# Kernel optimization log

Hardware: AMD Instinct MI355X
Metric: run time of the kernel (lower is better)

Reference implementation:

```python
import jax, jax.numpy as jnp
import numpy as np
import math

D_K = 64
ROUNDS = 4
BUCKET_LEN = 64


def _l2norm(x, axis):
    n = jnp.sqrt(jnp.sum(x * x, axis=axis, keepdims=True))
    return x / jnp.maximum(n, 1e-12)


def _look_back(x):
    # x: (B, n_buckets, bucket_len, ...) -> (B, n_buckets, 2*bucket_len, ...)
    # each bucket is concatenated with the previous bucket (wrapping at 0)
    shift = jnp.concatenate([x[:, -1:], x[:, :-1]], axis=1)
    return jnp.concatenate([shift, x], axis=2)


def _lsh_hash(query, rand_matrix):
    # returns position-tagged hashes: bucket_id * L + position, shape (B, L, R)
    B, L, D = query.shape
    qn = _l2norm(query, -1)
    rm = _l2norm(rand_matrix, 1)  # normalize over d_k dim, as in torch code
    xR = jnp.einsum('bld,bdrn->blrn', qn, rm)
    h = jnp.argmax(jnp.concatenate([xR, -xR], axis=-1), axis=-1).astype(jnp.int32)
    return h * L + jnp.arange(L, dtype=jnp.int32)[None, :, None]


def _attend(query, value, hash_indice, original_indice, sorted_hashes):
    B, L, D = query.shape
    nb = L // BUCKET_LEN
    R = ROUNDS
    # gather queries into hash-sorted order, per round: (B, L, D, R)
    rq = jnp.take_along_axis(query[:, :, :, None], hash_indice[:, :, None, :], axis=1)
    rq = rq.reshape(B, nb, BUCKET_LEN, D, R)
    lk = _l2norm(_look_back(rq), -2)  # keys = normalized lookback queries (shared QK)
    qk = jnp.einsum('bnijk,bnljk->bnilk', rq, lk) / math.sqrt(D_K)  # (B,nb,bl,2bl,R)
    # mask cross-bucket pairs
    sh = (sorted_hashes // L).reshape(B, nb, BUCKET_LEN, R)
    qk = jnp.where(sh[..., None, :] != _look_back(sh)[..., None, :, :], -1e9, qk)
    # mask self-attention (causal=False so no causal mask)
    qi = hash_indice.reshape(B, nb, BUCKET_LEN, R).astype(jnp.int32)
    ki = _look_back(qi)
    qk = jnp.where(qi[..., None, :] == ki[..., None, :, :], -1e5, qk)
    qk = qk.reshape(B, L, 2 * BUCKET_LEN, R)
    lse = jax.scipy.special.logsumexp(qk, axis=2)  # (B, L, R)
    p = jnp.exp(qk - lse[:, :, None, :]).reshape(B, nb, BUCKET_LEN, 2 * BUCKET_LEN, R)
    # gather values into sorted order and apply lookback attention
    rv = jnp.take_along_axis(value[:, :, :, None], hash_indice[:, :, None, :], axis=1)
    rv = rv.reshape(B, nb, BUCKET_LEN, D, R)
    att = jnp.einsum('bnijl,bnjkl->bnikl', p, _look_back(rv)).reshape(B, L, D, R)
    # scatter back to original order
    att = jnp.take_along_axis(att, original_indice[:, :, None, :], axis=1)
    lse = jnp.take_along_axis(lse, original_indice, axis=1)
    # NOTE: faithful to source, softmax over dim=1 (sequence dim)
    w = jax.nn.softmax(lse, axis=1)  # (B, L, R)
    return jnp.einsum('blir,blr->bli', att, w)  # (B, L, D)


def setup_inputs() -> dict:
    key = jax.random.key(0)
    k1, k2, k3 = jax.random.split(key, 3)
    B, L, D = 16, 8192, D_K
    n_buckets = L // BUCKET_LEN
    return {
        'query': jax.random.normal(k1, (B, L, D), jnp.float32),
        'value': jax.random.normal(k2, (B, L, D), jnp.float32),
        'rand_matrix': jax.random.normal(k3, (B, D, ROUNDS, n_buckets // 2), jnp.float32),
    }


def reference(query, value, rand_matrix):
    hashes = _lsh_hash(query, rand_matrix)          # (B, L, R) int32
    hash_indice = jnp.argsort(hashes, axis=1)       # sort positions by hash
    sorted_hashes = jnp.take_along_axis(hashes, hash_indice, axis=1)
    original_indice = jnp.argsort(hash_indice, axis=1)  # inverse permutation
    return _attend(query, value, hash_indice.astype(jnp.int32),
                   original_indice.astype(jnp.int32), sorted_hashes)
```

## Files before the change

### kernel.cpp

```cpp
#include <hip/hip_runtime.h>
#include <math.h>

#define B_   16
#define L_   8192
#define D_   64
#define R_   4
#define NB_  128
#define NH_  64

typedef float v2f __attribute__((ext_vector_type(2)));

__device__ __forceinline__ float dpp_xor1(float x) {
    return __int_as_float(__builtin_amdgcn_mov_dpp(__float_as_int(x), 0xB1, 0xf, 0xf, true));
}
__device__ __forceinline__ float dpp_xor2(float x) {
    return __int_as_float(__builtin_amdgcn_mov_dpp(__float_as_int(x), 0x4E, 0xf, 0xf, true));
}
__device__ __forceinline__ float quad_bcast0(float x) {
    return __int_as_float(__builtin_amdgcn_mov_dpp(__float_as_int(x), 0x00, 0xf, 0xf, true));
}
__device__ __forceinline__ float quad_bcast1(float x) {
    return __int_as_float(__builtin_amdgcn_mov_dpp(__float_as_int(x), 0x55, 0xf, 0xf, true));
}
__device__ __forceinline__ float quad_bcast2(float x) {
    return __int_as_float(__builtin_amdgcn_mov_dpp(__float_as_int(x), 0xAA, 0xf, 0xf, true));
}
__device__ __forceinline__ float quad_bcast3(float x) {
    return __int_as_float(__builtin_amdgcn_mov_dpp(__float_as_int(x), 0xFF, 0xf, 0xf, true));
}

__global__ __launch_bounds__(64) void k_rmnorm(const float* __restrict__ rm, double* __restrict__ rmn) {
    int b = blockIdx.x >> 2, r = blockIdx.x & 3;
    int n = threadIdx.x;
    float v[D_];
    double ss = 0.0;
    #pragma unroll
    for (int d = 0; d < D_; ++d) {
        float f = rm[((size_t)(b * D_ + d) * R_ + r) * NH_ + n];
        v[d] = f;
        ss += (double)f * (double)f;
    }
    double nrm = sqrt(ss); if (nrm < 1e-12) nrm = 1e-12;
    double inv = 1.0 / nrm;
    double* o = rmn + ((size_t)(b * R_ + r) * NH_ + n) * D_;
    #pragma unroll
    for (int d = 0; d < D_; ++d) o[d] = (double)v[d] * inv;
}

__global__ __launch_bounds__(256) void k_hash(const float* __restrict__ q, const double* __restrict__ rmn,
                                              float* __restrict__ rn, int* __restrict__ h) {
    __shared__ double rmd[NH_ * D_];
    __shared__ float  rms[NH_ * D_];
    int b = blockIdx.z, r = blockIdx.y;
    int l = blockIdx.x * 256 + threadIdx.x;
    const double* src = rmn + (size_t)(b * R_ + r) * NH_ * D_;
    for (int i = threadIdx.x; i < NH_ * D_; i += 256) {
        double dv = src[i];
        rmd[i] = dv;
        rms[i] = (float)dv;
    }
    const float* qp = q + ((size_t)b * L_ + l) * D_;
    v2f qv2[D_ / 2];
    double ss = 0.0;
    #pragma unroll
    for (int d = 0; d < D_; d += 4) {
        float4 f = *(const float4*)(qp + d);
        qv2[d >> 1]       = (v2f){f.x, f.y};
        qv2[(d >> 1) + 1] = (v2f){f.z, f.w};
        ss += (double)f.x * f.x + (double)f.y * f.y + (double)f.z * f.z + (double)f.w * f.w;
    }
    __syncthreads();
    float best = -1.0e30f, second = -1.0e30f; int bi = 0;
    for (int n = 0; n < NH_; ++n) {
        const float* kp = &rms[n * D_];
        v2f a0 = (v2f){0.f, 0.f}, a1 = a0;
        #pragma unroll
        for (int d = 0; d < D_; d += 4) {
            float4 kk = *(const float4*)(kp + d);
            a0 = __builtin_elementwise_fma(qv2[d >> 1],       (v2f){kk.x, kk.y}, a0);
            a1 = __builtin_elementwise_fma(qv2[(d >> 1) + 1], (v2f){kk.z, kk.w}, a1);
        }
        float s = (a0.x + a0.y) + (a1.x + a1.y);
        if (s > best)       { second = best; best = s; bi = n; }
        else if (s > second)  second = s;
        float ns = -s;
        if (ns > best)      { second = best; best = ns; bi = n + NH_; }
        else if (ns > second) second = ns;
    }
    float qn = (float)sqrt(ss);
    if (best - second < 1.2e-5f * qn + 1.0e-7f) {
        double qd[D_];
        #pragma unroll
        for (int d = 0; d < D_; d += 2) {
            qd[d] = (double)qv2[d >> 1].x; qd[d + 1] = (double)qv2[d >> 1].y;
        }
        double bestd = -1.0e300; bi = 0;
        for (int n = 0; n < NH_; ++n) {
            const double* kp = &rmd[n * D_];
            double a0 = 0, a1 = 0, a2 = 0, a3 = 0;
            #pragma unroll
            for (int d = 0; d < D_; d += 4) {
                a0 = fma(qd[d],   kp[d],   a0);
                a1 = fma(qd[d+1], kp[d+1], a1);
                a2 = fma(qd[d+2], kp[d+2], a2);
                a3 = fma(qd[d+3], kp[d+3], a3);
            }
            double s = (a0 + a1) + (a2 + a3);
            if (s > bestd)  { bestd = s;  bi = n; }
            if (-s > bestd) { bestd = -s; bi = n + NH_; }
        }
    }
    h[(size_t)(b * R_ + r) * L_ + l] = bi;
    if (r == 0) {
        double nrm = sqrt(ss); if (nrm < 1e-12) nrm = 1e-12;
        rn[(size_t)b * L_ + l] = (float)(1.0 / nrm);
    }
}

__global__ __launch_bounds__(64) void k_sort(const int* __restrict__ h, int* __restrict__ idx,
                                             int* __restrict__ sb, int* __restrict__ iv) {
    __shared__ unsigned int cnt[NB_ * 64];
    int br = blockIdx.x;
    const int* hh = h + (size_t)br * L_;
    int t = threadIdx.x;
    for (int i = t; i < NB_ * 64; i += 64) cnt[i] = 0;
    __syncthreads();
    int base = t * 128;
    for (int i = 0; i < 128; ++i) { int bk = hh[base + i]; cnt[bk * 64 + t]++; }
    __syncthreads();
    int fb = t * 128;
    unsigned int local = 0;
    for (int i = 0; i < 128; ++i) local += cnt[fb + i];
    unsigned int v = local;
    #pragma unroll
    for (int off = 1; off < 64; off <<= 1) {
        unsigned int u = __shfl_up(v, off);
        if (t >= off) v += u;
    }
    unsigned int run = v - local;
    for (int i = 0; i < 128; ++i) { unsigned int c0 = cnt[fb + i]; cnt[fb + i] = run; run += c0; }
    __syncthreads();
    int* oi = idx + (size_t)br * L_;
    int* ob = sb  + (size_t)br * L_;
    int* ivp = iv + (size_t)br * L_;
    for (int i = 0; i < 128; ++i) {
        int l = base + i; int bk = hh[l];
        unsigned int pos = cnt[bk * 64 + t]++;
        oi[pos] = l; ob[pos] = bk; ivp[l] = (int)pos;
    }
}

__global__ __launch_bounds__(128) void k_flash(const float* __restrict__ q, const float* __restrict__ val,
                                               const int* __restrict__ idx, const int* __restrict__ sb,
                                               const float* __restrict__ rn, float* __restrict__ lse,
                                               const float* __restrict__ gm, const float* __restrict__ gs,
                                               float* __restrict__ out, float* __restrict__ contrib,
                                               int r_fixed, int omode) {
    __shared__ float kt[2][16 * 80];
    __shared__ float vt[2][16 * 80];
    __shared__ int   kqs[2][16];
    __shared__ int   kbs[2][16];
    __shared__ float krs[2][16];
    int w   = threadIdx.x >> 6;
    int tid = threadIdx.x & 63;
    int c = blockIdx.x * 2 + w, b = blockIdx.z;
    int r = (r_fixed < 0) ? (int)blockIdx.y : r_fixed;
    size_t sbase = (size_t)(b * R_ + r) * L_;
    int h = tid & 3;
    int posq = c * 64 + (tid >> 2) * 4;
    int mls[4];
    #pragma unroll
    for (int qq = 0; qq < 4; ++qq) mls[qq] = idx[sbase + posq + qq];
    int ownpos  = posq + h;
    int myl_own = idx[sbase + ownpos];
    int mybk_own = sb[sbase + ownpos];
    float m_own = 0.125f / rn[(size_t)b * L_ + myl_own];
    const float* qb = q   + (size_t)b * L_ * D_;
    const float* vb = val + (size_t)b * L_ * D_;
    v2f qv2[4][8];
    #pragma unroll
    for (int qq = 0; qq < 4; ++qq) {
        const float* qp = qb + (size_t)mls[qq] * D_ + h * 16;
        #pragma unroll
        for (int i = 0; i < 16; i += 4) {
            float4 f = *(const float4*)(qp + i);
            qv2[qq][i >> 1]       = (v2f){f.x, f.y};
            qv2[qq][(i >> 1) + 1] = (v2f){f.z, f.w};
        }
    }
    float ps[4] = {0.0f, 0.0f, 0.0f, 0.0f};
    v2f acc2[4][8];
    #pragma unroll
    for (int qq = 0; qq < 4; ++qq)
        #pragma unroll
        for (int i = 0; i < 8; ++i) acc2[qq][i] = (v2f){0.0f, 0.0f};

    #pragma unroll 1
    for (int s = 0; s < 8; ++s) {
        int ck = ((c + NB_ - 1 + (s >> 2)) & (NB_ - 1)) * 64 + (s & 3) * 16;
        {
            int rw = tid >> 2, cc = tid & 3;
            int kl = idx[sbase + ck + rw];
            const float* kp = qb + (size_t)kl * D_ + cc * 16;
            float* kd = &kt[w][rw * 80 + cc * 20];
            #pragma unroll
            for (int i = 0; i < 16; i += 4) *(float4*)(kd + i) = *(const float4*)(kp + i);
            if (omode != 2) {
                const float* vp = vb + (size_t)kl * D_ + cc * 16;
                float* vd = &vt[w][rw * 80 + cc * 20];
                #pragma unroll
                for (int i = 0; i < 16; i += 4) *(float4*)(vd + i) = *(const float4*)(vp + i);
            }
            if (tid < 16) {
                int kl2 = idx[sbase + ck + tid];
                kqs[w][tid] = kl2;
                kbs[w][tid] = sb[sbase + ck + tid];
                krs[w][tid] = rn[(size_t)b * L_ + kl2] * 0.125f;
            }
        }
        #pragma unroll
        for (int j = 0; j < 16; ++j) {
            const float* kpj = &kt[w][j * 80 + h * 20];
            v2f a0 = (v2f){0.f, 0.f}, a1 = a0, a2 = a0, a3 = a0;
            #pragma unroll
            for (int i = 0; i < 16; i += 4) {
                float4 kk = *(const float4*)(kpj + i);
                v2f kA = (v2f){kk.x, kk.y}, kB = (v2f){kk.z, kk.w};
                int i2 = i >> 1;
                a0 = __builtin_elementwise_fma(qv2[0][i2], kA, a0);
                a0 = __builtin_elementwise_fma(qv2[0][i2 + 1], kB, a0);
                a1 = __builtin_elementwise_fma(qv2[1][i2], kA, a1);
                a1 = __builtin_elementwise_fma(qv2[1][i2 + 1], kB, a1);
                a2 = __builtin_elementwise_fma(qv2[2][i2], kA, a2);
                a2 = __builtin_elementwise_fma(qv2[2][i2 + 1], kB, a2);
                a3 = __builtin_elementwise_fma(qv2[3][i2], kA, a3);
                a3 = __builtin_elementwise_fma(qv2[3][i2 + 1], kB, a3);
            }
            float p0 = a0.x + a0.y, p1 = a1.x + a1.y, p2 = a2.x + a2.y, p3 = a3.x + a3.y;
            bool b0 = (h & 1), b1 = (h & 2) != 0;
            float u0 = b0 ? p1 : p0;
            float t0 = b0 ? p0 : p1;
            u0 += dpp_xor1(t0);
            float u2 = b0 ? p3 : p2;
            float t2 = b0 ? p2 : p3;
            u2 += dpp_xor1(t2);
            float dot = b1 ? u2 : u0;
            float t3 = b1 ? u0 : u2;
            dot += dpp_xor2(t3);
            float sc = dot * krs[w][j];
            sc = (kbs[w][j] == mybk_own) ? sc : -1.0e9f;
            if (kqs[w][j] == myl_own) sc = -1.0e5f;
            float p = __expf(sc - m_own);
            ps[j & 3] += p;
            if (omode != 2) {
                v2f P0 = (v2f){quad_bcast0(p), quad_bcast0(p)};
                v2f P1 = (v2f){quad_bcast1(p), quad_bcast1(p)};
                v2f P2 = (v2f){quad_bcast2(p), quad_bcast2(p)};
                v2f P3 = (v2f){quad_bcast3(p), quad_bcast3(p)};
                const float* vpj = &vt[w][j * 80 + h * 20];
                #pragma unroll
                for (int i = 0; i < 16; i += 4) {
                    float4 vv = *(const float4*)(vpj + i);
                    v2f vA = (v2f){vv.x, vv.y}, vB = (v2f){vv.z, vv.w};
                    int i2 = i >> 1;
                    acc2[0][i2]     = __builtin_elementwise_fma(P0, vA, acc2[0][i2]);
                    acc2[0][i2 + 1] = __builtin_elementwise_fma(P0, vB, acc2[0][i2 + 1]);
                    acc2[1][i2]     = __builtin_elementwise_fma(P1, vA, acc2[1][i2]);
                    acc2[1][i2 + 1] = __builtin_elementwise_fma(P1, vB, acc2[1][i2 + 1]);
                    acc2[2][i2]     = __builtin_elementwise_fma(P2, vA, acc2[2][i2]);
                    acc2[2][i2 + 1] = __builtin_elementwise_fma(P2, vB, acc2[2][i2 + 1]);
                    acc2[3][i2]     = __builtin_elementwise_fma(P3, vA, acc2[3][i2]);
                    acc2[3][i2 + 1] = __builtin_elementwise_fma(P3, vB, acc2[3][i2 + 1]);
                }
            }
        }
    }
    float sum = (ps[0] + ps[1]) + (ps[2] + ps[3]);
    float lse_own, inv_own;
    if (sum > 0.0f) { lse_own = m_own + logf(sum); inv_own = 1.0f / sum; }
    else            { lse_own = -3.0e38f;          inv_own = 0.0f; }
    if (omode != 3) lse[sbase + ownpos] = lse_own;
    if (omode == 0 || omode == 1) {
        float ivs[4];
        ivs[0] = quad_bcast0(inv_own); ivs[1] = quad_bcast1(inv_own);
        ivs[2] = quad_bcast2(inv_own); ivs[3] = quad_bcast3(inv_own);
        float* cbase = contrib + ((omode == 0) ? (size_t)(b * R_ + r) * L_ : (size_t)b * L_) * D_;
        #pragma unroll
        for (int qq = 0; qq < 4; ++qq) {
            float* cp = cbase + (size_t)(posq + qq) * D_ + h * 16;
            #pragma unroll
            for (int i = 0; i < 16; i += 4) {
                int i2 = i >> 1;
                float4 o;
                o.x = acc2[qq][i2].x * ivs[qq];     o.y = acc2[qq][i2].y * ivs[qq];
                o.z = acc2[qq][i2 + 1].x * ivs[qq]; o.w = acc2[qq][i2 + 1].y * ivs[qq];
                *(float4*)(cp + i) = o;
            }
        }
    } else if (omode == 3) {
        int brr = b * R_ + r;
        float gmv = gm[brr], gsv = gs[brr];
        float ls4[4], iv4[4];
        ls4[0] = quad_bcast0(lse_own); ls4[1] = quad_bcast1(lse_own);
        ls4[2] = quad_bcast2(lse_own); ls4[3] = quad_bcast3(lse_own);
        iv4[0] = quad_bcast0(inv_own); iv4[1] = quad_bcast1(inv_own);
        iv4[2] = quad_bcast2(inv_own); iv4[3] = quad_bcast3(inv_own);
        #pragma unroll
        for (int qq = 0; qq < 4; ++qq) {
            float wq = __expf(ls4[qq] - gmv) * gsv * iv4[qq];
            float* op = out + ((size_t)b * L_ + mls[qq]) * D_ + h * 16;
            #pragma unroll
            for (int i = 0; i < 8; ++i) {
                unsafeAtomicAdd(op + 2 * i,     wq * acc2[qq][i].x);
                unsafeAtomicAdd(op + 2 * i + 1, wq * acc2[qq][i].y);
            }
        }
    }
}

__global__ __launch_bounds__(256) void k_wred(const float* __restrict__ lse, float* __restrict__ gm,
                                              float* __restrict__ gs, int r_w) {
    __shared__ float  sm[4];
    __shared__ double sd[4];
    int br = (r_w < 0) ? (int)blockIdx.x : ((int)blockIdx.x * R_ + r_w);
    const float* x = lse + (size_t)br * L_;
    int t = threadIdx.x;
    float mx = -3.0e38f;
    for (int i = t; i < L_; i += 256) mx = fmaxf(mx, x[i]);
    #pragma unroll
    for (int o = 32; o; o >>= 1) mx = fmaxf(mx, __shfl_down(mx, o));
    if ((t & 63) == 0) sm[t >> 6] = mx;
    __syncthreads();
    mx = fmaxf(fmaxf(sm[0], sm[1]), fmaxf(sm[2], sm[3]));
    double s = 0.0;
    for (int i = t; i < L_; i += 256) s += exp((double)x[i] - (double)mx);
    #pragma unroll
    for (int o = 32; o; o >>= 1) s += __shfl_down(s, o);
    if ((t & 63) == 0) sd[t >> 6] = s;
    __syncthreads();
    if (t == 0) { gm[br] = mx; gs[br] = (float)(1.0 / (sd[0] + sd[1] + sd[2] + sd[3])); }
}

__global__ __launch_bounds__(256) void k_comb_full(const float* __restrict__ contrib,
                                                   const int* __restrict__ iv,
                                                   const float* __restrict__ lse,
                                                   const float* __restrict__ gm,
                                                   const float* __restrict__ gs,
                                                   float* __restrict__ out) {
    int gid = blockIdx.x * 256 + threadIdx.x;
    int row = gid >> 2;
    int ch  = (gid & 3) * 16;
    int b = row >> 13, l = row & (L_ - 1);
    float s[16];
    #pragma unroll
    for (int i = 0; i < 16; ++i) s[i] = 0.0f;
    #pragma unroll
    for (int r = 0; r < R_; ++r) {
        int brr = b * R_ + r;
        int pos = iv[(size_t)brr * L_ + l];
        float w = expf(lse[(size_t)brr * L_ + pos] - gm[brr]) * gs[brr];
        const float* cp = contrib + ((size_t)brr * L_ + pos) * D_ + ch;
        #pragma unroll
        for (int i = 0; i < 16; i += 4) {
            float4 f = *(const float4*)(cp + i);
            s[i]   = fmaf(w, f.x, s[i]);   s[i+1] = fmaf(w, f.y, s[i+1]);
            s[i+2] = fmaf(w, f.z, s[i+2]); s[i+3] = fmaf(w, f.w, s[i+3]);
        }
    }
    float* op = out + (size_t)row * D_ + ch;
    #pragma unroll
    for (int i = 0; i < 16; i += 4) {
        float4 o; o.x = s[i]; o.y = s[i+1]; o.z = s[i+2]; o.w = s[i+3];
        *(float4*)(op + i) = o;
    }
}

__global__ __launch_bounds__(256) void k_comb_add(const float* __restrict__ contrib,
                                                  const int* __restrict__ iv,
                                                  const float* __restrict__ lse,
                                                  const float* __restrict__ gm,
                                                  const float* __restrict__ gs,
                                                  float* __restrict__ out, int r) {
    int gid = blockIdx.x * 256 + threadIdx.x;
    int row = gid >> 2;
    int ch  = (gid & 3) * 16;
    int b = row >> 13, l = row & (L_ - 1);
    int brr = b * R_ + r;
    int pos = iv[(size_t)brr * L_ + l];
    float w = expf(lse[(size_t)brr * L_ + pos] - gm[brr]) * gs[brr];
    const float* cp = contrib + ((size_t)b * L_ + pos) * D_ + ch;
    float* op = out + (size_t)row * D_ + ch;
    #pragma unroll
    for (int i = 0; i < 16; i += 4) {
        float4 f = *(const float4*)(cp + i);
        float4 o = *(const float4*)(op + i);
        o.x = fmaf(w, f.x, o.x); o.y = fmaf(w, f.y, o.y);
        o.z = fmaf(w, f.z, o.z); o.w = fmaf(w, f.w, o.w);
        *(float4*)(op + i) = o;
    }
}

#define OFF_RMN     0u
#define OFF_RN      2097152u
#define OFF_H       2621440u
#define OFF_IDX     4718592u
#define OFF_SB      6815744u
#define OFF_LSE     8912896u
#define OFF_GM      11010048u
#define OFF_GS      11010304u
#define OFF_INV     11010560u
#define OFF_CONTRIB 13107712u
#define CONTRIB_FULL_BYTES  134217728ull
#define CONTRIB_SLICE_BYTES 33554432ull

extern "C" void kernel_launch(void* const* d_in, const int* in_sizes, int n_in,
                              void* d_out, int out_size, void* d_ws, size_t ws_size,
                              hipStream_t stream) {
    const float* q  = (const float*)d_in[0];
    const float* v  = (const float*)d_in[1];
    const float* rm = (const float*)d_in[2];
    float* out = (float*)d_out;
    char* ws = (char*)d_ws;
    double* rmn = (double*)(ws + OFF_RMN);
    float*  rn  = (float*)(ws + OFF_RN);
    int*    h   = (int*)(ws + OFF_H);
    int*    idx = (int*)(ws + OFF_IDX);
    int*    sb  = (int*)(ws + OFF_SB);
    float*  lse = (float*)(ws + OFF_LSE);
    float*  gm  = (float*)(ws + OFF_GM);
    float*  gs  = (float*)(ws + OFF_GS);
    int*    iv  = (int*)(ws + OFF_INV);
    float*  contrib = (float*)(ws + OFF_CONTRIB);

    int tierA = (ws_size >= (size_t)OFF_CONTRIB + CONTRIB_FULL_BYTES) ? 1 : 0;
    int tierB = (!tierA && ws_size >= (size_t)OFF_CONTRIB + CONTRIB_SLICE_BYTES) ? 1 : 0;

    hipLaunchKernelGGL(k_rmnorm, dim3(B_ * R_), dim3(64), 0, stream, rm, rmn);
    hipLaunchKernelGGL(k_hash, dim3(L_ / 256, R_, B_), dim3(256), 0, stream, q, rmn, rn, h);
    hipLaunchKernelGGL(k_sort, dim3(B_ * R_), dim3(64), 0, stream, h, idx, sb, iv);

    if (tierA) {
        hipLaunchKernelGGL(k_flash, dim3(NB_ / 2, R_, B_), dim3(128), 0, stream, q, v, idx, sb, rn,
                           lse, gm, gs, out, contrib, -1, 0);
        hipLaunchKernelGGL(k_wred, dim3(B_ * R_), dim3(256), 0, stream, lse, gm, gs, -1);
        hipLaunchKernelGGL(k_comb_full, dim3(B_ * L_ * 4 / 256), dim3(256), 0, stream,
                           contrib, iv, lse, gm, gs, out);
    } else if (tierB) {
        hipMemsetAsync(d_out, 0, (size_t)B_ * L_ * D_ * sizeof(float), stream);
        for (int r = 0; r < R_; ++r) {
            hipLaunchKernelGGL(k_flash, dim3(NB_ / 2, 1, B_), dim3(128), 0, stream, q, v, idx, sb, rn,
                               lse, gm, gs, out, contrib, r, 1);
            hipLaunchKernelGGL(k_wred, dim3(B_), dim3(256), 0, stream, lse, gm, gs, r);
            hipLaunchKernelGGL(k_comb_add, dim3(B_ * L_ * 4 / 256), dim3(256), 0, stream,
                               contrib, iv, lse, gm, gs, out, r);
        }
    } else {
        hipMemsetAsync(d_out, 0, (size_t)B_ * L_ * D_ * sizeof(float), stream);
        hipLaunchKernelGGL(k_flash, dim3(NB_ / 2, R_, B_), dim3(128), 0, stream, q, v, idx, sb, rn,
                           lse, gm, gs, out, contrib, -1, 2);
        hipLaunchKernelGGL(k_wred, dim3(B_ * R_), dim3(256), 0, stream, lse, gm, gs, -1);
        hipLaunchKernelGGL(k_flash, dim3(NB_ / 2, R_, B_), dim3(128), 0, stream, q, v, idx, sb, rn,
                           lse, gm, gs, out, contrib, -1, 3);
    }
}
```

Before: 556.4 us.

## Double-buffer key/value tiles via async global-to-LDS loads and widen sort

The flash kernel now runs one 64-thread block per bucket and prefetches the next 16-row key/value tile into the other LDS buffer with global_load_lds. Explicit vmcnt waits let that load overlap with compute on the current tile, and per-key metadata is precomputed once into LDS. The sort kernel uses 256 threads with padded counters and a cross-wave prefix scan, and the hash kernel drops its double-precision LDS copy so the rare fallback path reads from global memory. The risks are hand-written waitcnt correctness, LDS bank conflicts from the unpadded 64-float rows, and lower per-block occupancy.

```diff
diff --git a/kernel.cpp b/kernel.cpp
--- a/kernel.cpp
+++ b/kernel.cpp
@@ -29,6 +29,16 @@
     return __int_as_float(__builtin_amdgcn_mov_dpp(__float_as_int(x), 0xFF, 0xf, 0xf, true));
 }
 
+#define VMCNT8 asm volatile("s_waitcnt vmcnt(8)" ::: "memory")
+#define VMCNT4 asm volatile("s_waitcnt vmcnt(4)" ::: "memory")
+#define VMCNT0 asm volatile("s_waitcnt vmcnt(0)" ::: "memory")
+#define LGKM0  asm volatile("s_waitcnt lgkmcnt(0)" ::: "memory")
+
+__device__ __forceinline__ void gl_lds16(const float* g, float* l) {
+    __builtin_amdgcn_global_load_lds((const __attribute__((address_space(1))) void*)g,
+                                     (__attribute__((address_space(3))) void*)l, 16, 0, 0);
+}
+
 __global__ __launch_bounds__(64) void k_rmnorm(const float* __restrict__ rm, double* __restrict__ rmn) {
     int b = blockIdx.x >> 2, r = blockIdx.x & 3;
     int n = threadIdx.x;
@@ -49,16 +59,11 @@
 
 __global__ __launch_bounds__(256) void k_hash(const float* __restrict__ q, const double* __restrict__ rmn,
                                               float* __restrict__ rn, int* __restrict__ h) {
-    __shared__ double rmd[NH_ * D_];
-    __shared__ float  rms[NH_ * D_];
+    __shared__ float rms[NH_ * D_];
     int b = blockIdx.z, r = blockIdx.y;
     int l = blockIdx.x * 256 + threadIdx.x;
     const double* src = rmn + (size_t)(b * R_ + r) * NH_ * D_;
-    for (int i = threadIdx.x; i < NH_ * D_; i += 256) {
-        double dv = src[i];
-        rmd[i] = dv;
-        rms[i] = (float)dv;
-    }
+    for (int i = threadIdx.x; i < NH_ * D_; i += 256) rms[i] = (float)src[i];
     const float* qp = q + ((size_t)b * L_ + l) * D_;
     v2f qv2[D_ / 2];
     double ss = 0.0;
@@ -89,21 +94,16 @@
     }
     float qn = (float)sqrt(ss);
     if (best - second < 1.2e-5f * qn + 1.0e-7f) {
-        double qd[D_];
-        #pragma unroll
-        for (int d = 0; d < D_; d += 2) {
-            qd[d] = (double)qv2[d >> 1].x; qd[d + 1] = (double)qv2[d >> 1].y;
-        }
         double bestd = -1.0e300; bi = 0;
         for (int n = 0; n < NH_; ++n) {
-            const double* kp = &rmd[n * D_];
+            const double* kp = src + n * D_;
             double a0 = 0, a1 = 0, a2 = 0, a3 = 0;
             #pragma unroll
             for (int d = 0; d < D_; d += 4) {
-                a0 = fma(qd[d],   kp[d],   a0);
-                a1 = fma(qd[d+1], kp[d+1], a1);
-                a2 = fma(qd[d+2], kp[d+2], a2);
-                a3 = fma(qd[d+3], kp[d+3], a3);
+                a0 = fma((double)qv2[d >> 1].x,       kp[d],     a0);
+                a1 = fma((double)qv2[d >> 1].y,       kp[d + 1], a1);
+                a2 = fma((double)qv2[(d >> 1) + 1].x, kp[d + 2], a2);
+                a3 = fma((double)qv2[(d >> 1) + 1].y, kp[d + 3], a3);
             }
             double s = (a0 + a1) + (a2 + a3);
             if (s > bestd)  { bestd = s;  bi = n; }
@@ -117,55 +117,84 @@
     }
 }
 
-__global__ __launch_bounds__(64) void k_sort(const int* __restrict__ h, int* __restrict__ idx,
-                                             int* __restrict__ sb, int* __restrict__ iv) {
-    __shared__ unsigned int cnt[NB_ * 64];
+__global__ __launch_bounds__(256) void k_sort(const int* __restrict__ h, int* __restrict__ idx,
+                                              int* __restrict__ sb, int* __restrict__ iv) {
+    __shared__ unsigned int cnt[NB_ * 257];
+    __shared__ unsigned int wsum[4];
     int br = blockIdx.x;
     const int* hh = h + (size_t)br * L_;
     int t = threadIdx.x;
-    for (int i = t; i < NB_ * 64; i += 64) cnt[i] = 0;
-    __syncthreads();
-    int base = t * 128;
-    for (int i = 0; i < 128; ++i) { int bk = hh[base + i]; cnt[bk * 64 + t]++; }
+    for (int i = t; i < NB_ * 257; i += 256) cnt[i] = 0;
+    __syncthreads();
+    int base = t * 32;
+    for (int i = 0; i < 32; ++i) { int bk = hh[base + i]; cnt[bk * 257 + t]++; }
     __syncthreads();
     int fb = t * 128;
     unsigned int local = 0;
-    for (int i = 0; i < 128; ++i) local += cnt[fb + i];
+    for (int i = 0; i < 128; ++i) { unsigned g = fb + i; local += cnt[g + (g >> 8)]; }
     unsigned int v = local;
     #pragma unroll
     for (int off = 1; off < 64; off <<= 1) {
         unsigned int u = __shfl_up(v, off);
-        if (t >= off) v += u;
-    }
-    unsigned int run = v - local;
-    for (int i = 0; i < 128; ++i) { unsigned int c0 = cnt[fb + i]; cnt[fb + i] = run; run += c0; }
+        if ((t & 63) >= off) v += u;
+    }
+    if ((t & 63) == 63) wsum[t >> 6] = v;
+    __syncthreads();
+    unsigned int wbase = 0;
+    for (int w = 0; w < (t >> 6); ++w) wbase += wsum[w];
+    unsigned int run = wbase + v - local;
+    for (int i = 0; i < 128; ++i) {
+        unsigned g = fb + i;
+        unsigned int c0 = cnt[g + (g >> 8)];
+        cnt[g + (g >> 8)] = run; run += c0;
+    }
     __syncthreads();
     int* oi = idx + (size_t)br * L_;
     int* ob = sb  + (size_t)br * L_;
     int* ivp = iv + (size_t)br * L_;
-    for (int i = 0; i < 128; ++i) {
+    for (int i = 0; i < 32; ++i) {
         int l = base + i; int bk = hh[l];
-        unsigned int pos = cnt[bk * 64 + t]++;
+        unsigned int pos = cnt[bk * 257 + t]++;
         oi[pos] = l; ob[pos] = bk; ivp[l] = (int)pos;
     }
 }
 
-__global__ __launch_bounds__(128) void k_flash(const float* __restrict__ q, const float* __restrict__ val,
-                                               const int* __restrict__ idx, const int* __restrict__ sb,
-                                               const float* __restrict__ rn, float* __restrict__ lse,
-                                               const float* __restrict__ gm, const float* __restrict__ gs,
-                                               float* __restrict__ out, float* __restrict__ contrib,
-                                               int r_fixed, int omode) {
-    __shared__ float kt[2][16 * 80];
-    __shared__ float vt[2][16 * 80];
-    __shared__ int   kqs[2][16];
-    __shared__ int   kbs[2][16];
-    __shared__ float krs[2][16];
-    int w   = threadIdx.x >> 6;
-    int tid = threadIdx.x & 63;
-    int c = blockIdx.x * 2 + w, b = blockIdx.z;
+__device__ __forceinline__ void issue_stage(const float* qb, const float* vb,
+                                            const int4* krec, int kb16,
+                                            float* kd, float* vd, int tid, int loadv) {
+    #pragma unroll
+    for (int t4 = 0; t4 < 4; ++t4) {
+        int kl = krec[kb16 + t4 * 4 + (tid >> 4)].x;
+        size_t off = (size_t)kl * D_ + (size_t)((tid & 15) * 4);
+        gl_lds16(qb + off, kd + t4 * 256);
+        if (loadv) gl_lds16(vb + off, vd + t4 * 256);
+    }
+}
+
+__global__ __launch_bounds__(64) void k_flash(const float* __restrict__ q, const float* __restrict__ val,
+                                              const int* __restrict__ idx, const int* __restrict__ sb,
+                                              const float* __restrict__ rn, float* __restrict__ lse,
+                                              const float* __restrict__ gm, const float* __restrict__ gs,
+                                              float* __restrict__ out, float* __restrict__ contrib,
+                                              int r_fixed, int omode) {
+    __shared__ __align__(16) float kt[2][16 * 64];
+    __shared__ __align__(16) float vt[2][16 * 64];
+    __shared__ __align__(16) int4  krec[128];
+    int tid = threadIdx.x;
+    int c = blockIdx.x, b = blockIdx.z;
     int r = (r_fixed < 0) ? (int)blockIdx.y : r_fixed;
     size_t sbase = (size_t)(b * R_ + r) * L_;
+    int cprev = (c + NB_ - 1) & (NB_ - 1);
+    const float* qb = q   + (size_t)b * L_ * D_;
+    const float* vb = val + (size_t)b * L_ * D_;
+    int loadv = (omode != 2);
+    for (int t = tid; t < 128; t += 64) {
+        int pos = ((t < 64) ? cprev : c) * 64 + (t & 63);
+        int kl = idx[sbase + pos];
+        int kb = sb[sbase + pos];
+        float kr = rn[(size_t)b * L_ + kl] * 0.125f;
+        krec[t] = make_int4(kl, kb, __float_as_int(kr), 0);
+    }
     int h = tid & 3;
     int posq = c * 64 + (tid >> 2) * 4;
     int mls[4];
@@ -175,8 +204,6 @@
     int myl_own = idx[sbase + ownpos];
     int mybk_own = sb[sbase + ownpos];
     float m_own = 0.125f / rn[(size_t)b * L_ + myl_own];
-    const float* qb = q   + (size_t)b * L_ * D_;
-    const float* vb = val + (size_t)b * L_ * D_;
     v2f qv2[4][8];
     #pragma unroll
     for (int qq = 0; qq < 4; ++qq) {
@@ -195,32 +222,21 @@
         #pragma unroll
         for (int i = 0; i < 8; ++i) acc2[qq][i] = (v2f){0.0f, 0.0f};
 
+    LGKM0;
+    issue_stage(qb, vb, krec, 0, &kt[0][0], &vt[0][0], tid, loadv);
+
     #pragma unroll 1
     for (int s = 0; s < 8; ++s) {
-        int ck = ((c + NB_ - 1 + (s >> 2)) & (NB_ - 1)) * 64 + (s & 3) * 16;
-        {
-            int rw = tid >> 2, cc = tid & 3;
-            int kl = idx[sbase + ck + rw];
-            const float* kp = qb + (size_t)kl * D_ + cc * 16;
-            float* kd = &kt[w][rw * 80 + cc * 20];
-            #pragma unroll
-            for (int i = 0; i < 16; i += 4) *(float4*)(kd + i) = *(const float4*)(kp + i);
-            if (omode != 2) {
-                const float* vp = vb + (size_t)kl * D_ + cc * 16;
-                float* vd = &vt[w][rw * 80 + cc * 20];
-                #pragma unroll
-                for (int i = 0; i < 16; i += 4) *(float4*)(vd + i) = *(const float4*)(vp + i);
-            }
-            if (tid < 16) {
-                int kl2 = idx[sbase + ck + tid];
-                kqs[w][tid] = kl2;
-                kbs[w][tid] = sb[sbase + ck + tid];
-                krs[w][tid] = rn[(size_t)b * L_ + kl2] * 0.125f;
-            }
-        }
-        #pragma unroll
+        const float* ktp = &kt[s & 1][0];
+        const float* vtp = &vt[s & 1][0];
+        LGKM0;
+        if (s < 7)
+            issue_stage(qb, vb, krec, (s + 1) * 16, &kt[(s + 1) & 1][0], &vt[(s + 1) & 1][0], tid, loadv);
+        if (s < 7) { if (loadv) { VMCNT8; } else { VMCNT4; } } else { VMCNT0; }
+        __builtin_amdgcn_sched_barrier(0);
         for (int j = 0; j < 16; ++j) {
-            const float* kpj = &kt[w][j * 80 + h * 20];
+            int4 kv = krec[s * 16 + j];
+            const float* kpj = ktp + j * 64 + h * 16;
             v2f a0 = (v2f){0.f, 0.f}, a1 = a0, a2 = a0, a3 = a0;
             #pragma unroll
             for (int i = 0; i < 16; i += 4) {
@@ -247,9 +263,9 @@
             float dot = b1 ? u2 : u0;
             float t3 = b1 ? u0 : u2;
             dot += dpp_xor2(t3);
-            float sc = dot * krs[w][j];
-            sc = (kbs[w][j] == mybk_own) ? sc : -1.0e9f;
-            if (kqs[w][j] == myl_own) sc = -1.0e5f;
+            float sc = dot * __int_as_float(kv.z);
+            sc = (kv.y == mybk_own) ? sc : -1.0e9f;
+            if (kv.x == myl_own) sc = -1.0e5f;
             float p = __expf(sc - m_own);
             ps[j & 3] += p;
             if (omode != 2) {
@@ -257,7 +273,7 @@
                 v2f P1 = (v2f){quad_bcast1(p), quad_bcast1(p)};
                 v2f P2 = (v2f){quad_bcast2(p), quad_bcast2(p)};
                 v2f P3 = (v2f){quad_bcast3(p), quad_bcast3(p)};
-                const float* vpj = &vt[w][j * 80 + h * 20];
+                const float* vpj = vtp + j * 64 + h * 16;
                 #pragma unroll
                 for (int i = 0; i < 16; i += 4) {
                     float4 vv = *(const float4*)(vpj + i);
@@ -437,10 +453,10 @@
 
     hipLaunchKernelGGL(k_rmnorm, dim3(B_ * R_), dim3(64), 0, stream, rm, rmn);
     hipLaunchKernelGGL(k_hash, dim3(L_ / 256, R_, B_), dim3(256), 0, stream, q, rmn, rn, h);
-    hipLaunchKernelGGL(k_sort, dim3(B_ * R_), dim3(64), 0, stream, h, idx, sb, iv);
+    hipLaunchKernelGGL(k_sort, dim3(B_ * R_), dim3(256), 0, stream, h, idx, sb, iv);
 
     if (tierA) {
-        hipLaunchKernelGGL(k_flash, dim3(NB_ / 2, R_, B_), dim3(128), 0, stream, q, v, idx, sb, rn,
+        hipLaunchKernelGGL(k_flash, dim3(NB_, R_, B_), dim3(64), 0, stream, q, v, idx, sb, rn,
                            lse, gm, gs, out, contrib, -1, 0);
         hipLaunchKernelGGL(k_wred, dim3(B_ * R_), dim3(256), 0, stream, lse, gm, gs, -1);
         hipLaunchKernelGGL(k_comb_full, dim3(B_ * L_ * 4 / 256), dim3(256), 0, stream,
@@ -448,7 +464,7 @@
     } else if (tierB) {
         hipMemsetAsync(d_out, 0, (size_t)B_ * L_ * D_ * sizeof(float), stream);
         for (int r = 0; r < R_; ++r) {
-            hipLaunchKernelGGL(k_flash, dim3(NB_ / 2, 1, B_), dim3(128), 0, stream, q, v, idx, sb, rn,
+            hipLaunchKernelGGL(k_flash, dim3(NB_, 1, B_), dim3(64), 0, stream, q, v, idx, sb, rn,
                                lse, gm, gs, out, contrib, r, 1);
             hipLaunchKernelGGL(k_wred, dim3(B_), dim3(256), 0, stream, lse, gm, gs, r);
             hipLaunchKernelGGL(k_comb_add, dim3(B_ * L_ * 4 / 256), dim3(256), 0, stream,
@@ -456,10 +472,10 @@
         }
     } else {
         hipMemsetAsync(d_out, 0, (size_t)B_ * L_ * D_ * sizeof(float), stream);
-        hipLaunchKernelGGL(k_flash, dim3(NB_ / 2, R_, B_), dim3(128), 0, stream, q, v, idx, sb, rn,
+        hipLaunchKernelGGL(k_flash, dim3(NB_, R_, B_), dim3(64), 0, stream, q, v, idx, sb, rn,
                            lse, gm, gs, out, contrib, -1, 2);
         hipLaunchKernelGGL(k_wred, dim3(B_ * R_), dim3(256), 0, stream, lse, gm, gs, -1);
-        hipLaunchKernelGGL(k_flash, dim3(NB_ / 2, R_, B_), dim3(128), 0, stream, q, v, idx, sb, rn,
+        hipLaunchKernelGGL(k_flash, dim3(NB_, R_, B_), dim3(64), 0, stream, q, v, idx, sb, rn,
                            lse, gm, gs, out, contrib, -1, 3);
     }
 }
```

Result: no change. 561.1 us (+0.9%).
